# Performance work log

Measured on AMD Instinct MI355X. Metric: run time of the kernel, lower is better.

The kernel has to match this reference:

```python
import jax, jax.numpy as jnp
import numpy as np

C = 6.5  # ALCOVE specificity constant

BATCH, NE, NDIMS = 2048, 2048, 128


def setup_inputs() -> dict:
    key = jax.random.key(0)
    k1, k2, k3 = jax.random.split(key, 3)
    inputs = jax.random.normal(k1, (BATCH, NDIMS), dtype=jnp.float32)
    exemplars = jax.random.normal(k2, (NE, NDIMS), dtype=jnp.float32)
    # attn initialized to ones/ndims in the original; use positive random values
    # scaled similarly so the exp argument stays in a reasonable range.
    attn = jax.random.uniform(k3, (NDIMS,), dtype=jnp.float32) / float(NDIMS)
    return {"inputs": inputs, "exemplars": exemplars, "attn": attn}


def reference(inputs, exemplars, attn):
    # Vectorized form of: exp(-c * sum_d attn_d * |exemplars - x|) per example.
    # diff: (batch, ne, ndims)
    diff = jnp.abs(exemplars[None, :, :] - inputs[:, None, :])
    dist = jnp.einsum('bed,d->be', diff, attn)  # weighted L1 distance
    return jnp.exp(-C * dist)  # (batch, ne)
```

## Files before the change

kernel.cpp:

```cpp
#include <hip/hip_runtime.h>
#include <stdint.h>


#define BATCH 2048
#define NE 2048
#define ND 128

#define TILE 64
#define KC 64

#define QSCALE 16777216.0f
#define QBIAS  2097152.5f
#define KEXP   (-6.5f / 16777216.0f)

#define SAD(acc, a, b) asm("v_sad_u32 %0, %1, %2, %0" : "+v"(acc) : "v"(a), "v"(b))

__device__ __forceinline__ void qwrite(uint32_t* __restrict__ Xs,
                                       uint32_t* __restrict__ Es,
                                       const float4* fx, const float4* fe,
                                       float4 s, int c4, int rr, int swk) {
#pragma unroll
  for (int t = 0; t < 16; ++t) {
    const int wb = (4 * c4) * TILE + (((t ^ swk) << 2) + rr);
    Xs[wb + 0 * TILE] = (uint32_t)fmaf(fx[t].x, s.x, QBIAS);
    Xs[wb + 1 * TILE] = (uint32_t)fmaf(fx[t].y, s.y, QBIAS);
    Xs[wb + 2 * TILE] = (uint32_t)fmaf(fx[t].z, s.z, QBIAS);
    Xs[wb + 3 * TILE] = (uint32_t)fmaf(fx[t].w, s.w, QBIAS);
    Es[wb + 0 * TILE] = (uint32_t)fmaf(fe[t].x, s.x, QBIAS);
    Es[wb + 1 * TILE] = (uint32_t)fmaf(fe[t].y, s.y, QBIAS);
    Es[wb + 2 * TILE] = (uint32_t)fmaf(fe[t].z, s.z, QBIAS);
    Es[wb + 3 * TILE] = (uint32_t)fmaf(fe[t].w, s.w, QBIAS);
  }
}

__device__ __forceinline__ void compute_chunk(const uint32_t* __restrict__ Xs,
                                              const uint32_t* __restrict__ Es,
                                              int by, int ex, uint32_t acc[8][8]) {
  const uint4* Xs4 = (const uint4*)Xs;
  const uint4* Es4 = (const uint4*)Es;
#pragma unroll 2
  for (int d4 = 0; d4 < KC; d4 += 4) {
    const int sw = (d4 >> 2) & 7;
    const uint4* xp = Xs4 + d4 * (TILE / 4) + (by ^ sw);
    const uint4* ep = Es4 + d4 * (TILE / 4) + (ex ^ sw);
#pragma unroll
    for (int j = 0; j < 4; ++j) {
      uint4 xa = xp[j * 16];
      uint4 xb = xp[j * 16 + 8];
      uint4 ea = ep[j * 16];
      uint4 eb = ep[j * 16 + 8];
      uint32_t xv[8] = {xa.x, xa.y, xa.z, xa.w, xb.x, xb.y, xb.z, xb.w};
      uint32_t ev[8] = {ea.x, ea.y, ea.z, ea.w, eb.x, eb.y, eb.z, eb.w};
#pragma unroll
      for (int i = 0; i < 8; ++i)
#pragma unroll
        for (int k = 0; k < 8; ++k) SAD(acc[i][k], xv[i], ev[k]);
    }
  }
}

__global__ __launch_bounds__(64, 1)
void alcove_rbf_kernel(const float* __restrict__ X,
                       const float* __restrict__ E,
                       const float* __restrict__ A,
                       float* __restrict__ out) {
  __shared__ uint32_t Xs[KC * TILE];
  __shared__ uint32_t Es[KC * TILE];

  const int tid = (int)threadIdx.x;
  const int e0 = (int)blockIdx.x * TILE;
  const int b0 = (int)blockIdx.y * TILE;

  const int ex = tid & 7;
  const int by = tid >> 3;
  const int c4 = tid & 15;
  const int rr = tid >> 4;
  const int swk = c4 & 7;

  uint32_t acc[8][8];
#pragma unroll
  for (int i = 0; i < 8; ++i)
#pragma unroll
    for (int k = 0; k < 8; ++k) acc[i][k] = 0u;

  const float* xbase = X + (size_t)(b0 + rr) * ND + 4 * c4;
  const float* ebase = E + (size_t)(e0 + rr) * ND + 4 * c4;

  float4 a0 = ((const float4*)A)[c4];
  float4 a1 = ((const float4*)(A + KC))[c4];
  float4 s0, s1;
  s0.x = a0.x * QSCALE; s0.y = a0.y * QSCALE; s0.z = a0.z * QSCALE; s0.w = a0.w * QSCALE;
  s1.x = a1.x * QSCALE; s1.y = a1.y * QSCALE; s1.z = a1.z * QSCALE; s1.w = a1.w * QSCALE;

  float4 f0x[16], f0e[16];
#pragma unroll
  for (int t = 0; t < 16; ++t) {
    f0x[t] = *(const float4*)(xbase + (size_t)(4 * t) * ND);
    f0e[t] = *(const float4*)(ebase + (size_t)(4 * t) * ND);
  }
  qwrite(Xs, Es, f0x, f0e, s0, c4, rr, swk);

  float4 f1x[16], f1e[16];
#pragma unroll
  for (int t = 0; t < 16; ++t) {
    f1x[t] = *(const float4*)(xbase + (size_t)(4 * t) * ND + KC);
    f1e[t] = *(const float4*)(ebase + (size_t)(4 * t) * ND + KC);
  }

  compute_chunk(Xs, Es, by, ex, acc);

  qwrite(Xs, Es, f1x, f1e, s1, c4, rr, swk);

  compute_chunk(Xs, Es, by, ex, acc);

#pragma unroll
  for (int i = 0; i < 8; ++i) {
    const int b = b0 + 4 * by + (i & 3) + ((i >> 2) << 5);
    float* orow = out + (size_t)b * NE + e0;
    float4 oA, oB;
    oA.x = __expf(KEXP * (float)acc[i][0]);
    oA.y = __expf(KEXP * (float)acc[i][1]);
    oA.z = __expf(KEXP * (float)acc[i][2]);
    oA.w = __expf(KEXP * (float)acc[i][3]);
    oB.x = __expf(KEXP * (float)acc[i][4]);
    oB.y = __expf(KEXP * (float)acc[i][5]);
    oB.z = __expf(KEXP * (float)acc[i][6]);
    oB.w = __expf(KEXP * (float)acc[i][7]);
    *(float4*)(orow + 4 * ex) = oA;
    *(float4*)(orow + 32 + 4 * ex) = oB;
  }
}

extern "C" void kernel_launch(void* const* d_in, const int* in_sizes, int n_in,
                              void* d_out, int out_size, void* d_ws, size_t ws_size,
                              hipStream_t stream) {
  const float* X = (const float*)d_in[0];
  const float* E = (const float*)d_in[1];
  const float* A = (const float*)d_in[2];
  float* out = (float*)d_out;

  dim3 grid(NE / TILE, BATCH / TILE);
  dim3 block(64);
  alcove_rbf_kernel<<<grid, block, 0, stream>>>(X, E, A, out);
}
```

Measured before the change: 85.77 us.

## Split reduction dimension across four waves per block with LDS reduction

Expands each block from one wave to four, with each wave accumulating SAD partial sums over a quarter of the feature dimension for the same 64x64 tile. Partial accumulators are combined through a two-step LDS tree reduction, and two waves then apply exp and store. The shared-memory layout becomes row-major with an XOR swizzle, and loads are spread across all threads. This is intended to raise occupancy and latency hiding, at the cost of extra barriers, LDS reduction traffic and loss of register prefetching of the second chunk.

New measurement: 88.31 us. 3.0% more time.

```diff
diff --git a/kernel.cpp b/kernel.cpp
--- a/kernel.cpp
+++ b/kernel.cpp
@@ -15,67 +15,22 @@
 
 #define SAD(acc, a, b) asm("v_sad_u32 %0, %1, %2, %0" : "+v"(acc) : "v"(a), "v"(b))
 
-__device__ __forceinline__ void qwrite(uint32_t* __restrict__ Xs,
-                                       uint32_t* __restrict__ Es,
-                                       const float4* fx, const float4* fe,
-                                       float4 s, int c4, int rr, int swk) {
-#pragma unroll
-  for (int t = 0; t < 16; ++t) {
-    const int wb = (4 * c4) * TILE + (((t ^ swk) << 2) + rr);
-    Xs[wb + 0 * TILE] = (uint32_t)fmaf(fx[t].x, s.x, QBIAS);
-    Xs[wb + 1 * TILE] = (uint32_t)fmaf(fx[t].y, s.y, QBIAS);
-    Xs[wb + 2 * TILE] = (uint32_t)fmaf(fx[t].z, s.z, QBIAS);
-    Xs[wb + 3 * TILE] = (uint32_t)fmaf(fx[t].w, s.w, QBIAS);
-    Es[wb + 0 * TILE] = (uint32_t)fmaf(fe[t].x, s.x, QBIAS);
-    Es[wb + 1 * TILE] = (uint32_t)fmaf(fe[t].y, s.y, QBIAS);
-    Es[wb + 2 * TILE] = (uint32_t)fmaf(fe[t].z, s.z, QBIAS);
-    Es[wb + 3 * TILE] = (uint32_t)fmaf(fe[t].w, s.w, QBIAS);
-  }
-}
-
-__device__ __forceinline__ void compute_chunk(const uint32_t* __restrict__ Xs,
-                                              const uint32_t* __restrict__ Es,
-                                              int by, int ex, uint32_t acc[8][8]) {
-  const uint4* Xs4 = (const uint4*)Xs;
-  const uint4* Es4 = (const uint4*)Es;
-#pragma unroll 2
-  for (int d4 = 0; d4 < KC; d4 += 4) {
-    const int sw = (d4 >> 2) & 7;
-    const uint4* xp = Xs4 + d4 * (TILE / 4) + (by ^ sw);
-    const uint4* ep = Es4 + d4 * (TILE / 4) + (ex ^ sw);
-#pragma unroll
-    for (int j = 0; j < 4; ++j) {
-      uint4 xa = xp[j * 16];
-      uint4 xb = xp[j * 16 + 8];
-      uint4 ea = ep[j * 16];
-      uint4 eb = ep[j * 16 + 8];
-      uint32_t xv[8] = {xa.x, xa.y, xa.z, xa.w, xb.x, xb.y, xb.z, xb.w};
-      uint32_t ev[8] = {ea.x, ea.y, ea.z, ea.w, eb.x, eb.y, eb.z, eb.w};
-#pragma unroll
-      for (int i = 0; i < 8; ++i)
-#pragma unroll
-        for (int k = 0; k < 8; ++k) SAD(acc[i][k], xv[i], ev[k]);
-    }
-  }
-}
-
-__global__ __launch_bounds__(64, 1)
+__global__ __launch_bounds__(256, 4)
 void alcove_rbf_kernel(const float* __restrict__ X,
                        const float* __restrict__ E,
                        const float* __restrict__ A,
                        float* __restrict__ out) {
-  __shared__ uint32_t Xs[KC * TILE];
-  __shared__ uint32_t Es[KC * TILE];
+  __shared__ uint32_t Xs[TILE * KC];
+  __shared__ uint32_t Es[TILE * KC];
 
   const int tid = (int)threadIdx.x;
+  const int wv = tid >> 6;
+  const int lane = tid & 63;
   const int e0 = (int)blockIdx.x * TILE;
   const int b0 = (int)blockIdx.y * TILE;
 
-  const int ex = tid & 7;
-  const int by = tid >> 3;
-  const int c4 = tid & 15;
-  const int rr = tid >> 4;
-  const int swk = c4 & 7;
+  const int ex = lane & 7;
+  const int by = lane >> 3;
 
   uint32_t acc[8][8];
 #pragma unroll
@@ -83,51 +38,142 @@
 #pragma unroll
     for (int k = 0; k < 8; ++k) acc[i][k] = 0u;
 
-  const float* xbase = X + (size_t)(b0 + rr) * ND + 4 * c4;
-  const float* ebase = E + (size_t)(e0 + rr) * ND + 4 * c4;
+  const float4* A4 = (const float4*)A;
 
-  float4 a0 = ((const float4*)A)[c4];
-  float4 a1 = ((const float4*)(A + KC))[c4];
-  float4 s0, s1;
-  s0.x = a0.x * QSCALE; s0.y = a0.y * QSCALE; s0.z = a0.z * QSCALE; s0.w = a0.w * QSCALE;
-  s1.x = a1.x * QSCALE; s1.y = a1.y * QSCALE; s1.z = a1.z * QSCALE; s1.w = a1.w * QSCALE;
+  for (int kc = 0; kc < ND; kc += KC) {
+    if (kc) __syncthreads();
 
-  float4 f0x[16], f0e[16];
 #pragma unroll
-  for (int t = 0; t < 16; ++t) {
-    f0x[t] = *(const float4*)(xbase + (size_t)(4 * t) * ND);
-    f0e[t] = *(const float4*)(ebase + (size_t)(4 * t) * ND);
-  }
-  qwrite(Xs, Es, f0x, f0e, s0, c4, rr, swk);
+    for (int t = 0; t < 4; ++t) {
+      const int slot = t * 256 + tid;
+      const int row = slot >> 4;
+      const int blk = slot & 15;
+      const float4 a = A4[(kc >> 2) + blk];
+      const float sx = a.x * QSCALE, sy = a.y * QSCALE,
+                  sz = a.z * QSCALE, sw = a.w * QSCALE;
+      const float4 vx = *(const float4*)(X + (size_t)(b0 + row) * ND + kc + 4 * blk);
+      const float4 ve = *(const float4*)(E + (size_t)(e0 + row) * ND + kc + 4 * blk);
+      const int w = row * KC + ((4 * blk) ^ (((row >> 2) & 7) << 2));
+      uint4 qx, qe;
+      qx.x = (uint32_t)fmaf(vx.x, sx, QBIAS);
+      qx.y = (uint32_t)fmaf(vx.y, sy, QBIAS);
+      qx.z = (uint32_t)fmaf(vx.z, sz, QBIAS);
+      qx.w = (uint32_t)fmaf(vx.w, sw, QBIAS);
+      qe.x = (uint32_t)fmaf(ve.x, sx, QBIAS);
+      qe.y = (uint32_t)fmaf(ve.y, sy, QBIAS);
+      qe.z = (uint32_t)fmaf(ve.z, sz, QBIAS);
+      qe.w = (uint32_t)fmaf(ve.w, sw, QBIAS);
+      *(uint4*)(Xs + w) = qx;
+      *(uint4*)(Es + w) = qe;
+    }
+    __syncthreads();
 
-  float4 f1x[16], f1e[16];
 #pragma unroll
-  for (int t = 0; t < 16; ++t) {
-    f1x[t] = *(const float4*)(xbase + (size_t)(4 * t) * ND + KC);
-    f1e[t] = *(const float4*)(ebase + (size_t)(4 * t) * ND + KC);
+    for (int u = 0; u < 4; ++u) {
+      const int d4 = 16 * wv + 4 * u;
+      const uint32_t* xp = Xs + (d4 ^ (by << 2));
+      const uint32_t* ep = Es + (d4 ^ (ex << 2));
+      uint4 xr[8];
+#pragma unroll
+      for (int j = 0; j < 4; ++j) {
+        xr[j]     = *(const uint4*)(xp + (4 * by + j) * KC);
+        xr[4 + j] = *(const uint4*)(xp + (4 * by + j + 32) * KC);
+      }
+#pragma unroll
+      for (int kk = 0; kk < 8; ++kk) {
+        const int er = 4 * ex + (kk & 3) + ((kk >> 2) << 5);
+        const uint4 ev = *(const uint4*)(ep + er * KC);
+#pragma unroll
+        for (int i = 0; i < 8; ++i) {
+          SAD(acc[i][kk], xr[i].x, ev.x);
+          SAD(acc[i][kk], xr[i].y, ev.y);
+          SAD(acc[i][kk], xr[i].z, ev.z);
+          SAD(acc[i][kk], xr[i].w, ev.w);
+        }
+      }
+    }
   }
 
-  compute_chunk(Xs, Es, by, ex, acc);
+  uint32_t* PA = Xs;
+  uint32_t* PB = Es;
+  __syncthreads();
+  if (wv == 1) {
+#pragma unroll
+    for (int i = 0; i < 8; ++i) {
+      *(uint4*)(PA + ((2 * i) * 64 + lane) * 4) =
+          make_uint4(acc[i][0], acc[i][1], acc[i][2], acc[i][3]);
+      *(uint4*)(PA + ((2 * i + 1) * 64 + lane) * 4) =
+          make_uint4(acc[i][4], acc[i][5], acc[i][6], acc[i][7]);
+    }
+  } else if (wv == 3) {
+#pragma unroll
+    for (int i = 0; i < 8; ++i) {
+      *(uint4*)(PB + ((2 * i) * 64 + lane) * 4) =
+          make_uint4(acc[i][0], acc[i][1], acc[i][2], acc[i][3]);
+      *(uint4*)(PB + ((2 * i + 1) * 64 + lane) * 4) =
+          make_uint4(acc[i][4], acc[i][5], acc[i][6], acc[i][7]);
+    }
+  }
+  __syncthreads();
+  if (wv == 0) {
+#pragma unroll
+    for (int i = 0; i < 8; ++i) {
+      uint4 pa = *(const uint4*)(PA + ((2 * i) * 64 + lane) * 4);
+      uint4 pb = *(const uint4*)(PA + ((2 * i + 1) * 64 + lane) * 4);
+      acc[i][0] += pa.x; acc[i][1] += pa.y; acc[i][2] += pa.z; acc[i][3] += pa.w;
+      acc[i][4] += pb.x; acc[i][5] += pb.y; acc[i][6] += pb.z; acc[i][7] += pb.w;
+    }
+#pragma unroll
+    for (int i = 4; i < 8; ++i) {
+      *(uint4*)(PA + (((i - 4) * 2) * 64 + lane) * 4) =
+          make_uint4(acc[i][0], acc[i][1], acc[i][2], acc[i][3]);
+      *(uint4*)(PA + (((i - 4) * 2 + 1) * 64 + lane) * 4) =
+          make_uint4(acc[i][4], acc[i][5], acc[i][6], acc[i][7]);
+    }
+  } else if (wv == 2) {
+#pragma unroll
+    for (int i = 0; i < 8; ++i) {
+      uint4 pa = *(const uint4*)(PB + ((2 * i) * 64 + lane) * 4);
+      uint4 pb = *(const uint4*)(PB + ((2 * i + 1) * 64 + lane) * 4);
+      acc[i][0] += pa.x; acc[i][1] += pa.y; acc[i][2] += pa.z; acc[i][3] += pa.w;
+      acc[i][4] += pb.x; acc[i][5] += pb.y; acc[i][6] += pb.z; acc[i][7] += pb.w;
+    }
+#pragma unroll
+    for (int i = 0; i < 4; ++i) {
+      *(uint4*)(PB + ((i * 2) * 64 + lane) * 4) =
+          make_uint4(acc[i][0], acc[i][1], acc[i][2], acc[i][3]);
+      *(uint4*)(PB + ((i * 2 + 1) * 64 + lane) * 4) =
+          make_uint4(acc[i][4], acc[i][5], acc[i][6], acc[i][7]);
+    }
+  }
+  __syncthreads();
 
-  qwrite(Xs, Es, f1x, f1e, s1, c4, rr, swk);
-
-  compute_chunk(Xs, Es, by, ex, acc);
-
+  if (wv == 0 || wv == 2) {
+    const int ibase = (wv == 0) ? 0 : 4;
+    const uint32_t* P = (wv == 0) ? PB : PA;
 #pragma unroll
-  for (int i = 0; i < 8; ++i) {
-    const int b = b0 + 4 * by + (i & 3) + ((i >> 2) << 5);
-    float* orow = out + (size_t)b * NE + e0;
-    float4 oA, oB;
-    oA.x = __expf(KEXP * (float)acc[i][0]);
-    oA.y = __expf(KEXP * (float)acc[i][1]);
-    oA.z = __expf(KEXP * (float)acc[i][2]);
-    oA.w = __expf(KEXP * (float)acc[i][3]);
-    oB.x = __expf(KEXP * (float)acc[i][4]);
-    oB.y = __expf(KEXP * (float)acc[i][5]);
-    oB.z = __expf(KEXP * (float)acc[i][6]);
-    oB.w = __expf(KEXP * (float)acc[i][7]);
-    *(float4*)(orow + 4 * ex) = oA;
-    *(float4*)(orow + 32 + 4 * ex) = oB;
+    for (int q = 0; q < 4; ++q) {
+      const int i = ibase + q;
+      uint4 pa = *(const uint4*)(P + ((q * 2) * 64 + lane) * 4);
+      uint4 pb = *(const uint4*)(P + ((q * 2 + 1) * 64 + lane) * 4);
+      const uint32_t s0 = acc[i][0] + pa.x, s1 = acc[i][1] + pa.y;
+      const uint32_t s2 = acc[i][2] + pa.z, s3 = acc[i][3] + pa.w;
+      const uint32_t s4 = acc[i][4] + pb.x, s5 = acc[i][5] + pb.y;
+      const uint32_t s6 = acc[i][6] + pb.z, s7 = acc[i][7] + pb.w;
+      const int b = b0 + 4 * by + (i & 3) + ((i >> 2) << 5);
+      float* orow = out + (size_t)b * NE + e0;
+      float4 oA, oB;
+      oA.x = __expf(KEXP * (float)s0);
+      oA.y = __expf(KEXP * (float)s1);
+      oA.z = __expf(KEXP * (float)s2);
+      oA.w = __expf(KEXP * (float)s3);
+      oB.x = __expf(KEXP * (float)s4);
+      oB.y = __expf(KEXP * (float)s5);
+      oB.z = __expf(KEXP * (float)s6);
+      oB.w = __expf(KEXP * (float)s7);
+      *(float4*)(orow + 4 * ex) = oA;
+      *(float4*)(orow + 32 + 4 * ex) = oB;
+    }
   }
 }
 
@@ -140,6 +186,6 @@
   float* out = (float*)d_out;
 
   dim3 grid(NE / TILE, BATCH / TILE);
-  dim3 block(64);
+  dim3 block(256);
   alcove_rbf_kernel<<<grid, block, 0, stream>>>(X, E, A, out);
 }
```
